# Optimization experiments

Hardware: AMD Instinct MI355X
Metric: run time of the kernel (lower is better)

The kernel has to match this reference:

```python
import jax, jax.numpy as jnp
import numpy as np

HIDDEN = 512
B, H, W = 8, 48, 48
SCALE = 1.0 / np.sqrt(HIDDEN).astype(np.float32)


def conv1x1(x, w, b):
    # x: [B, C, H, W], w: [O, C], b: [O]  (1x1 Conv2d == channel matmul)
    return jnp.einsum('bchw,oc->bohw', x, w) + b[None, :, None, None]


def setup_inputs() -> dict:
    key = jax.random.key(0)
    ks = jax.random.split(key, 10)
    s = 1.0 / np.sqrt(HIDDEN)
    return {
        'locx': jax.random.normal(ks[0], (B, HIDDEN, H, W), dtype=jnp.float32),
        'glox': jax.random.normal(ks[1], (B, HIDDEN, H, W), dtype=jnp.float32),
        'Wq': jax.random.normal(ks[2], (HIDDEN, HIDDEN), dtype=jnp.float32) * s,
        'bq': jax.random.normal(ks[3], (HIDDEN,), dtype=jnp.float32) * 0.01,
        'Wk': jax.random.normal(ks[4], (HIDDEN, HIDDEN), dtype=jnp.float32) * s,
        'bk': jax.random.normal(ks[5], (HIDDEN,), dtype=jnp.float32) * 0.01,
        'Wv': jax.random.normal(ks[6], (HIDDEN, HIDDEN), dtype=jnp.float32) * s,
        'bv': jax.random.normal(ks[7], (HIDDEN,), dtype=jnp.float32) * 0.01,
        'Wo': jax.random.normal(ks[8], (HIDDEN, HIDDEN), dtype=jnp.float32) * s,
        'bo': jax.random.normal(ks[9], (HIDDEN,), dtype=jnp.float32) * 0.01,
    }


def reference(locx, glox, Wq, bq, Wk, bk, Wv, bv, Wo, bo):
    b, c, h, w = locx.shape
    # 1x1 conv projections
    q = conv1x1(locx, Wq, bq).reshape(b, c, h * w)   # [B, C, N]
    k = conv1x1(glox, Wk, bk).reshape(b, c, -1)      # [B, C, M]
    v = conv1x1(glox, Wv, bv).reshape(b, c, -1)      # [B, C, M]
    # scores = Q^T K / sqrt(hidden)  -> [B, N, M]
    scores = jnp.einsum('bcn,bcm->bnm', q, k) * SCALE
    probs = jax.nn.softmax(scores, axis=-1)           # dropout rate 0.0 -> identity
    # context = probs @ V^T -> [B, N, C] -> [B, C, H, H]
    ctx = jnp.einsum('bnm,bcm->bcn', probs, v).reshape(b, c, h, h)
    out = conv1x1(ctx, Wo, bo)                        # proj dropout 0.0 -> identity
    return out
```

## Files before the change

### kernel.cpp

```cpp
#include <hip/hip_runtime.h>
#include <hip/hip_bf16.h>

typedef __attribute__((ext_vector_type(4))) float f32x4;
typedef __attribute__((ext_vector_type(8))) short bf16x8;
typedef __attribute__((ext_vector_type(4))) short s16x4;

#define C_DIM 512
#define N_PIX 2304
#define N_BATCH 8
#define ATT_SCALE 0.04419417382415922f
#define NJB 18

typedef __attribute__((address_space(3))) unsigned int lds_u32;
typedef const __attribute__((address_space(1))) unsigned int glob_u32;

__device__ __forceinline__ void gl2lds16(const __hip_bfloat16* g, __hip_bfloat16* l)
{
    __builtin_amdgcn_global_load_lds((glob_u32*)g, (lds_u32*)l, 16, 0, 0);
}

template<int OUT_BF16, int BIAS_MODE, int EPI, int MERGE2, int NJ, int NS>
__global__ __launch_bounds__(256)
void gemm_bt(const __hip_bfloat16* __restrict__ A0, const __hip_bfloat16* __restrict__ B0,
             void* __restrict__ D0, const float* __restrict__ bias0,
             float* __restrict__ rsum,
             const __hip_bfloat16* __restrict__ A1, const __hip_bfloat16* __restrict__ B1,
             void* __restrict__ D1, const float* __restrict__ bias1,
             float scale, int K, int lda, int ldb, int ldd,
             long sA, long sB, long sD)
{
    __shared__ __hip_bfloat16 As[128 * 64];
    __shared__ __hip_bfloat16 Bs[128 * 64];

    const int lin = blockIdx.x;
    const int s   = lin % NS;
    const int t   = lin / NS;
    const int bz  = MERGE2 ? (s & 7) : s;
    const int jb  = t % NJ;
    const int j0  = jb * 128;
    const int i0  = (t / NJ) * 128;

    const __hip_bfloat16* A = A0;
    const __hip_bfloat16* B = B0;
    void* Dp = (void*)D0;
    const float* bias = bias0;
    if (MERGE2 && (s >> 3)) { A = A1; B = B1; Dp = D1; bias = bias1; }

    const int tid  = threadIdx.x;
    const int lane = tid & 63;
    const int wave = tid >> 6;

    const __hip_bfloat16* Ab = A + (size_t)bz * (size_t)sA;
    const __hip_bfloat16* Bb = B + (size_t)bz * (size_t)sB;
    __hip_bfloat16* D16 = (__hip_bfloat16*)Dp + (size_t)bz * (size_t)sD;
    float*          D32 = (float*)Dp          + (size_t)bz * (size_t)sD;

    const int lrow = lane >> 3;
    const int lcs  = (lane & 7) ^ lrow;
    const __hip_bfloat16* ga = Ab + (size_t)(i0 + wave * 32 + lrow) * lda + lcs * 8;
    const __hip_bfloat16* gb = Bb + (size_t)(j0 + wave * 32 + lrow) * ldb + lcs * 8;
    __hip_bfloat16* la = As + wave * 32 * 64;
    __hip_bfloat16* lb = Bs + wave * 32 * 64;

    const int fr = lane & 15;
    const int fq = lane >> 4;
    const int sw = fr & 7;
    const int wi = (wave >> 1) * 64;
    const int wj = (wave & 1) * 64;

    f32x4 acc[4][4];
#pragma unroll
    for (int a = 0; a < 4; ++a)
#pragma unroll
        for (int b = 0; b < 4; ++b)
            acc[a][b] = (f32x4){0.f, 0.f, 0.f, 0.f};

    for (int k0 = 0; k0 < K; k0 += 64) {
#pragma unroll
        for (int ss = 0; ss < 4; ++ss) {
            gl2lds16(ga + (size_t)ss * 8 * lda + k0, la + ss * 8 * 64);
            gl2lds16(gb + (size_t)ss * 8 * ldb + k0, lb + ss * 8 * 64);
        }
        __syncthreads();

#pragma unroll
        for (int kk = 0; kk < 2; ++kk) {
            bf16x8 af[4], bfr[4];
            const int ca = ((kk * 4 + fq) ^ sw) << 3;
#pragma unroll
            for (int tt = 0; tt < 4; ++tt) {
                af[tt]  = *(const bf16x8*)(&As[(wi + tt * 16 + fr) * 64 + ca]);
                bfr[tt] = *(const bf16x8*)(&Bs[(wj + tt * 16 + fr) * 64 + ca]);
            }
#pragma unroll
            for (int a = 0; a < 4; ++a)
#pragma unroll
                for (int b = 0; b < 4; ++b)
                    acc[a][b] = __builtin_amdgcn_mfma_f32_16x16x32_bf16(
                        af[a], bfr[b], acc[a][b], 0, 0, 0);
        }
        __syncthreads();
    }

    const int orow = fq * 4;

    float inv[4][4];
    if (EPI == 2) {
        const float* ri = rsum + (size_t)bz * N_PIX;
#pragma unroll
        for (int a = 0; a < 4; ++a)
#pragma unroll
            for (int r = 0; r < 4; ++r)
                inv[a][r] = ri[i0 + wi + a * 16 + orow + r];
    }

    float rpart[4][4];
    if (EPI == 1) {
#pragma unroll
        for (int a = 0; a < 4; ++a)
#pragma unroll
            for (int r = 0; r < 4; ++r)
                rpart[a][r] = 0.f;
    }

#pragma unroll
    for (int a = 0; a < 4; ++a) {
        int ib = i0 + wi + a * 16 + orow;
#pragma unroll
        for (int b = 0; b < 4; ++b) {
            int j = j0 + wj + b * 16 + fr;
            float bj = (BIAS_MODE == 2) ? bias[j] : 0.f;
#pragma unroll
            for (int r = 0; r < 4; ++r) {
                int i = ib + r;
                float v = acc[a][b][r] * scale;
                if (BIAS_MODE == 1) v += bias[i];
                if (BIAS_MODE == 2) v += bj;
                if (EPI == 1) { v = __expf(v); rpart[a][r] += v; }
                if (EPI == 2) v *= inv[a][r];
                if (OUT_BF16)
                    D16[(size_t)i * ldd + j] = __float2bfloat16(v);
                else
                    D32[(size_t)i * ldd + j] = v;
            }
        }
    }

    if (EPI == 1) {
#pragma unroll
        for (int m = 1; m < 16; m <<= 1)
#pragma unroll
            for (int a = 0; a < 4; ++a)
#pragma unroll
                for (int r = 0; r < 4; ++r)
                    rpart[a][r] += __shfl_xor(rpart[a][r], m);
        float* rsl = (float*)As;
        if (fr == 0) {
#pragma unroll
            for (int a = 0; a < 4; ++a)
#pragma unroll
                for (int r = 0; r < 4; ++r)
                    rsl[wave * 64 + a * 16 + orow + r] = rpart[a][r];
        }
        __syncthreads();
        if (tid < 128) {
            int half = tid >> 6, rr = tid & 63;
            float sm = rsl[(half * 2) * 64 + rr] + rsl[(half * 2 + 1) * 64 + rr];
            rsum[((size_t)jb * N_BATCH + bz) * N_PIX + i0 + tid] = sm;
        }
    }
}

__global__ __launch_bounds__(256)
void reduce_rinv(const float* __restrict__ rp, float* __restrict__ rinv)
{
    int idx = blockIdx.x * 256 + threadIdx.x;
    float s = 0.f;
#pragma unroll
    for (int jb = 0; jb < NJB; ++jb)
        s += rp[(size_t)jb * N_BATCH * N_PIX + idx];
    rinv[idx] = 1.f / s;
}

__global__ __launch_bounds__(256)
void transpose_cast(const float* __restrict__ X, __hip_bfloat16* __restrict__ Xt)
{
    __shared__ float t[64 * 65];
    const int n0 = blockIdx.x * 64;
    const int c0 = blockIdx.y * 64;
    const size_t b = blockIdx.z;
    const float* Xb = X + b * (size_t)C_DIM * N_PIX;
    const int tid = threadIdx.x;

    const int n_l = tid & 63;
    const int c_b = tid >> 6;
#pragma unroll
    for (int s = 0; s < 16; ++s) {
        int c_l = c_b + s * 4;
        t[c_l * 65 + n_l] = Xb[(size_t)(c0 + c_l) * N_PIX + n0 + n_l];
    }
    __syncthreads();

    const int cc = (tid & 7) * 8;
    const int nb = tid >> 3;
#pragma unroll
    for (int it = 0; it < 2; ++it) {
        int n2 = nb + it * 32;
        union { __hip_bfloat16 h[8]; int4 v; } u;
#pragma unroll
        for (int w = 0; w < 8; ++w)
            u.h[w] = __float2bfloat16(t[(cc + w) * 65 + n2]);
        *(int4*)(&Xt[((size_t)b * N_PIX + n0 + n2) * C_DIM + c0 + cc]) = u.v;
    }
}

__global__ __launch_bounds__(256)
void cast_w4(const float* __restrict__ s0, const float* __restrict__ s1,
             const float* __restrict__ s2, const float* __restrict__ s3,
             __hip_bfloat16* __restrict__ dst)
{
    const float* srcs[4] = {s0, s1, s2, s3};
    const int w = blockIdx.y;
    const int i = (blockIdx.x * 256 + threadIdx.x) * 4;
    float4 f = *(const float4*)(srcs[w] + i);
    union { __hip_bfloat16 h[4]; s16x4 q; } t;
    t.h[0] = __float2bfloat16(f.x);
    t.h[1] = __float2bfloat16(f.y);
    t.h[2] = __float2bfloat16(f.z);
    t.h[3] = __float2bfloat16(f.w);
    *(s16x4*)(dst + (size_t)w * C_DIM * C_DIM + i) = t.q;
}

extern "C" void kernel_launch(void* const* d_in, const int* in_sizes, int n_in,
                              void* d_out, int out_size, void* d_ws, size_t ws_size,
                              hipStream_t stream)
{
    const float* locx = (const float*)d_in[0];
    const float* glox = (const float*)d_in[1];
    const float* Wq = (const float*)d_in[2];
    const float* bq = (const float*)d_in[3];
    const float* Wk = (const float*)d_in[4];
    const float* bk = (const float*)d_in[5];
    const float* Wv = (const float*)d_in[6];
    const float* bv = (const float*)d_in[7];
    const float* Wo = (const float*)d_in[8];
    const float* bo = (const float*)d_in[9];
    float* out = (float*)d_out;

    const int C = C_DIM, N = N_PIX;
    const size_t WB   = (size_t)C * C * 2;
    const size_t szX  = (size_t)N_BATCH * N * C * 2;
    const size_t szP1 = (size_t)N * N * 2;
    const size_t szRP = (size_t)NJB * N_BATCH * N * 4;
    const size_t szRI = (size_t)N_BATCH * N * 4;

    const size_t fixed = 4 * WB + 6 * szX + szRP + szRI;
    bool full = (ws_size >= fixed + 8 * szP1 + 8 * 256);

    char* ws = (char*)d_ws;
    size_t off = 0;
    auto alloc = [&](size_t bytes) {
        char* p = ws + off;
        off += (bytes + 255) & ~(size_t)255;
        return p;
    };
    __hip_bfloat16* wgt = (__hip_bfloat16*)alloc(4 * WB);
    __hip_bfloat16* Xl  = (__hip_bfloat16*)alloc(szX);
    __hip_bfloat16* Xg  = (__hip_bfloat16*)alloc(szX);
    __hip_bfloat16* Qt  = (__hip_bfloat16*)alloc(szX);
    __hip_bfloat16* Kt  = (__hip_bfloat16*)alloc(szX);
    __hip_bfloat16* Vb  = (__hip_bfloat16*)alloc(szX);
    __hip_bfloat16* Ctx = (__hip_bfloat16*)alloc(szX);
    float*          rp   = (float*)alloc(szRP);
    float*          rinv = (float*)alloc(szRI);
    __hip_bfloat16* Pu  = (__hip_bfloat16*)alloc(full ? 8 * szP1 : szP1);

    __hip_bfloat16* wq_b = wgt;
    __hip_bfloat16* wk_b = wgt + (size_t)C * C;
    __hip_bfloat16* wv_b = wgt + 2 * (size_t)C * C;
    __hip_bfloat16* wo_b = wgt + 3 * (size_t)C * C;

    const dim3 blk(256);
    const long sPr = (long)N * C;
    const long sV  = (long)C * N;

    cast_w4<<<dim3(C * C / 1024, 4), blk, 0, stream>>>(Wq, Wk, Wv, Wo, wgt);
    transpose_cast<<<dim3(N / 64, C / 64, 8), blk, 0, stream>>>(locx, Xl);
    transpose_cast<<<dim3(N / 64, C / 64, 8), blk, 0, stream>>>(glox, Xg);

    gemm_bt<1, 2, 0, 1, 4, 16><<<dim3(18 * 4 * 16), blk, 0, stream>>>(
        Xl, wq_b, Qt, bq, nullptr, Xg, wk_b, Kt, bk,
        1.f, C, C, C, C, sPr, 0, sPr);
    gemm_bt<1, 1, 0, 0, 18, 8><<<dim3(4 * 18 * 8), blk, 0, stream>>>(
        wv_b, Xg, Vb, bv, nullptr, nullptr, nullptr, nullptr, nullptr,
        1.f, C, C, C, N, 0, sPr, sV);

    if (full) {
        gemm_bt<1, 0, 1, 0, 18, 8><<<dim3(18 * 18 * 8), blk, 0, stream>>>(
            Qt, Kt, Pu, nullptr, rp, nullptr, nullptr, nullptr, nullptr,
            ATT_SCALE, C, C, C, N, sPr, sPr, (long)N * N);
        reduce_rinv<<<dim3(8 * N / 256), blk, 0, stream>>>(rp, rinv);
        gemm_bt<1, 0, 2, 0, 4, 8><<<dim3(18 * 4 * 8), blk, 0, stream>>>(
            Pu, Vb, Ctx, nullptr, rinv, nullptr, nullptr, nullptr, nullptr,
            1.f, N, N, N, C, (long)N * N, sV, sPr);
    } else {
        for (int r = 0; r < N_BATCH; ++r) {
            gemm_bt<1, 0, 1, 0, 18, 1><<<dim3(18 * 18), blk, 0, stream>>>(
                Qt + (size_t)r * sPr, Kt + (size_t)r * sPr, Pu, nullptr,
                rp + (size_t)r * N, nullptr, nullptr, nullptr, nullptr,
                ATT_SCALE, C, C, C, N, 0, 0, 0);
            reduce_rinv<<<dim3(N / 256), blk, 0, stream>>>(
                rp + (size_t)r * N, rinv + (size_t)r * N);
            gemm_bt<1, 0, 2, 0, 4, 1><<<dim3(18 * 4), blk, 0, stream>>>(
                Pu, Vb + (size_t)r * sV, Ctx + (size_t)r * sPr, nullptr,
                rinv + (size_t)r * N, nullptr, nullptr, nullptr, nullptr,
                1.f, N, N, N, C, 0, 0, 0);
        }
    }

    gemm_bt<0, 1, 0, 0, 18, 8><<<dim3(4 * 18 * 8), blk, 0, stream>>>(
        wo_b, Ctx, out, bo, nullptr, nullptr, nullptr, nullptr, nullptr,
        1.f, C, C, C, N, 0, sPr, (long)C * N);
}
```

Measured before the change: 368.2 us.

## Fold output projection into V before attention and fuse QKV projections

Uses associativity so Wo is applied to V first (Vp = Wo·V), and the final GEMM computes out = Vp·P^T with column-wise softmax normalization and bias applied in the epilogue. This removes the separate Ctx buffer and the final projection GEMM over the attention output. Q, K and V projections are merged into one kernel, and both input transposes run in a single launch, cutting launch count. Normalization now happens after the Wo product, which changes rounding order, and the P·V GEMM now writes fp32 output directly.

```diff
diff --git a/kernel.cpp b/kernel.cpp
--- a/kernel.cpp
+++ b/kernel.cpp
@@ -19,13 +19,11 @@
     __builtin_amdgcn_global_load_lds((glob_u32*)g, (lds_u32*)l, 16, 0, 0);
 }
 
-template<int OUT_BF16, int BIAS_MODE, int EPI, int MERGE2, int NJ, int NS>
+template<int OUT_BF16, int BIAS_MODE, int EPI, int NJ, int NS, int IFAST, int NI>
 __global__ __launch_bounds__(256)
-void gemm_bt(const __hip_bfloat16* __restrict__ A0, const __hip_bfloat16* __restrict__ B0,
-             void* __restrict__ D0, const float* __restrict__ bias0,
+void gemm_bt(const __hip_bfloat16* __restrict__ A, const __hip_bfloat16* __restrict__ B,
+             void* __restrict__ Dp, const float* __restrict__ bias,
              float* __restrict__ rsum,
-             const __hip_bfloat16* __restrict__ A1, const __hip_bfloat16* __restrict__ B1,
-             void* __restrict__ D1, const float* __restrict__ bias1,
              float scale, int K, int lda, int ldb, int ldd,
              long sA, long sB, long sD)
 {
@@ -35,16 +33,12 @@
     const int lin = blockIdx.x;
     const int s   = lin % NS;
     const int t   = lin / NS;
-    const int bz  = MERGE2 ? (s & 7) : s;
-    const int jb  = t % NJ;
-    const int j0  = jb * 128;
-    const int i0  = (t / NJ) * 128;
-
-    const __hip_bfloat16* A = A0;
-    const __hip_bfloat16* B = B0;
-    void* Dp = (void*)D0;
-    const float* bias = bias0;
-    if (MERGE2 && (s >> 3)) { A = A1; B = B1; Dp = D1; bias = bias1; }
+    const int bz  = s;
+    int ib, jb;
+    if (IFAST) { ib = t % NI; jb = t / NI; }
+    else       { jb = t % NJ; ib = t / NJ; }
+    const int i0 = ib * 128;
+    const int j0 = jb * 128;
 
     const int tid  = threadIdx.x;
     const int lane = tid & 63;
@@ -104,14 +98,12 @@
 
     const int orow = fq * 4;
 
-    float inv[4][4];
-    if (EPI == 2) {
+    float rjv[4];
+    if (EPI == 3) {
         const float* ri = rsum + (size_t)bz * N_PIX;
 #pragma unroll
-        for (int a = 0; a < 4; ++a)
-#pragma unroll
-            for (int r = 0; r < 4; ++r)
-                inv[a][r] = ri[i0 + wi + a * 16 + orow + r];
+        for (int b = 0; b < 4; ++b)
+            rjv[b] = ri[j0 + wj + b * 16 + fr];
     }
 
     float rpart[4][4];
@@ -125,19 +117,19 @@
 
 #pragma unroll
     for (int a = 0; a < 4; ++a) {
-        int ib = i0 + wi + a * 16 + orow;
+        int ibx = i0 + wi + a * 16 + orow;
 #pragma unroll
         for (int b = 0; b < 4; ++b) {
             int j = j0 + wj + b * 16 + fr;
             float bj = (BIAS_MODE == 2) ? bias[j] : 0.f;
 #pragma unroll
             for (int r = 0; r < 4; ++r) {
-                int i = ib + r;
+                int i = ibx + r;
                 float v = acc[a][b][r] * scale;
+                if (EPI == 3) v *= rjv[b];
                 if (BIAS_MODE == 1) v += bias[i];
                 if (BIAS_MODE == 2) v += bj;
                 if (EPI == 1) { v = __expf(v); rpart[a][r] += v; }
-                if (EPI == 2) v *= inv[a][r];
                 if (OUT_BF16)
                     D16[(size_t)i * ldd + j] = __float2bfloat16(v);
                 else
@@ -172,6 +164,96 @@
 }
 
 __global__ __launch_bounds__(256)
+void proj_qkv(const __hip_bfloat16* __restrict__ Xl,
+              const __hip_bfloat16* __restrict__ Xg,
+              const __hip_bfloat16* __restrict__ wgt,
+              const float* __restrict__ bq, const float* __restrict__ bk,
+              const float* __restrict__ bv,
+              __hip_bfloat16* __restrict__ QKV)
+{
+    __shared__ __hip_bfloat16 As[128 * 64];
+    __shared__ __hip_bfloat16 Bs[128 * 64];
+
+    const int lin = blockIdx.x;
+    const int s   = lin % 24;
+    const int bz  = s & 7;
+    const int mat = s >> 3;
+    const int t   = lin / 24;
+    const int j0  = (t & 3) * 128;
+    const int i0  = (t >> 2) * 128;
+
+    const __hip_bfloat16* Ab = ((mat == 0) ? Xl : Xg) + (size_t)bz * N_PIX * C_DIM;
+    const __hip_bfloat16* Bb = wgt + (size_t)mat * C_DIM * C_DIM;
+    const float* bias = (mat == 0) ? bq : (mat == 1) ? bk : bv;
+    __hip_bfloat16* D = QKV + ((size_t)mat * N_BATCH + bz) * N_PIX * C_DIM;
+
+    const int tid  = threadIdx.x;
+    const int lane = tid & 63;
+    const int wave = tid >> 6;
+
+    const int lrow = lane >> 3;
+    const int lcs  = (lane & 7) ^ lrow;
+    const __hip_bfloat16* ga = Ab + (size_t)(i0 + wave * 32 + lrow) * C_DIM + lcs * 8;
+    const __hip_bfloat16* gb = Bb + (size_t)(j0 + wave * 32 + lrow) * C_DIM + lcs * 8;
+    __hip_bfloat16* la = As + wave * 32 * 64;
+    __hip_bfloat16* lb = Bs + wave * 32 * 64;
+
+    const int fr = lane & 15;
+    const int fq = lane >> 4;
+    const int sw = fr & 7;
+    const int wi = (wave >> 1) * 64;
+    const int wj = (wave & 1) * 64;
+
+    f32x4 acc[4][4];
+#pragma unroll
+    for (int a = 0; a < 4; ++a)
+#pragma unroll
+        for (int b = 0; b < 4; ++b)
+            acc[a][b] = (f32x4){0.f, 0.f, 0.f, 0.f};
+
+    for (int k0 = 0; k0 < C_DIM; k0 += 64) {
+#pragma unroll
+        for (int ss = 0; ss < 4; ++ss) {
+            gl2lds16(ga + (size_t)ss * 8 * C_DIM + k0, la + ss * 8 * 64);
+            gl2lds16(gb + (size_t)ss * 8 * C_DIM + k0, lb + ss * 8 * 64);
+        }
+        __syncthreads();
+
+#pragma unroll
+        for (int kk = 0; kk < 2; ++kk) {
+            bf16x8 af[4], bfr[4];
+            const int ca = ((kk * 4 + fq) ^ sw) << 3;
+#pragma unroll
+            for (int tt = 0; tt < 4; ++tt) {
+                af[tt]  = *(const bf16x8*)(&As[(wi + tt * 16 + fr) * 64 + ca]);
+                bfr[tt] = *(const bf16x8*)(&Bs[(wj + tt * 16 + fr) * 64 + ca]);
+            }
+#pragma unroll
+            for (int a = 0; a < 4; ++a)
+#pragma unroll
+                for (int b = 0; b < 4; ++b)
+                    acc[a][b] = __builtin_amdgcn_mfma_f32_16x16x32_bf16(
+                        af[a], bfr[b], acc[a][b], 0, 0, 0);
+        }
+        __syncthreads();
+    }
+
+    const int orow = fq * 4;
+#pragma unroll
+    for (int a = 0; a < 4; ++a) {
+        int ibx = i0 + wi + a * 16 + orow;
+#pragma unroll
+        for (int b = 0; b < 4; ++b) {
+            int j = j0 + wj + b * 16 + fr;
+            float bj = bias[j];
+#pragma unroll
+            for (int r = 0; r < 4; ++r)
+                D[(size_t)(ibx + r) * C_DIM + j] = __float2bfloat16(acc[a][b][r] + bj);
+        }
+    }
+}
+
+__global__ __launch_bounds__(256)
 void reduce_rinv(const float* __restrict__ rp, float* __restrict__ rinv)
 {
     int idx = blockIdx.x * 256 + threadIdx.x;
@@ -183,13 +265,16 @@
 }
 
 __global__ __launch_bounds__(256)
-void transpose_cast(const float* __restrict__ X, __hip_bfloat16* __restrict__ Xt)
+void transpose_cast(const float* __restrict__ locx, const float* __restrict__ glox,
+                    __hip_bfloat16* __restrict__ Xl, __hip_bfloat16* __restrict__ Xg)
 {
     __shared__ float t[64 * 65];
     const int n0 = blockIdx.x * 64;
     const int c0 = blockIdx.y * 64;
-    const size_t b = blockIdx.z;
-    const float* Xb = X + b * (size_t)C_DIM * N_PIX;
+    const int z  = blockIdx.z;
+    const size_t b = z & 7;
+    const float* Xb = ((z < 8) ? locx : glox) + b * (size_t)C_DIM * N_PIX;
+    __hip_bfloat16* Xt = (z < 8) ? Xl : Xg;
     const int tid = threadIdx.x;
 
     const int n_l = tid & 63;
@@ -210,7 +295,7 @@
 #pragma unroll
         for (int w = 0; w < 8; ++w)
             u.h[w] = __float2bfloat16(t[(cc + w) * 65 + n2]);
-        *(int4*)(&Xt[((size_t)b * N_PIX + n0 + n2) * C_DIM + c0 + cc]) = u.v;
+        *(int4*)(&Xt[(b * N_PIX + n0 + n2) * C_DIM + c0 + cc]) = u.v;
     }
 }
 
@@ -255,7 +340,7 @@
     const size_t szRI = (size_t)N_BATCH * N * 4;
 
     const size_t fixed = 4 * WB + 6 * szX + szRP + szRI;
-    bool full = (ws_size >= fixed + 8 * szP1 + 8 * 256);
+    bool full = (ws_size >= fixed + 8 * szP1 + 4096);
 
     char* ws = (char*)d_ws;
     size_t off = 0;
@@ -267,58 +352,52 @@
     __hip_bfloat16* wgt = (__hip_bfloat16*)alloc(4 * WB);
     __hip_bfloat16* Xl  = (__hip_bfloat16*)alloc(szX);
     __hip_bfloat16* Xg  = (__hip_bfloat16*)alloc(szX);
-    __hip_bfloat16* Qt  = (__hip_bfloat16*)alloc(szX);
-    __hip_bfloat16* Kt  = (__hip_bfloat16*)alloc(szX);
-    __hip_bfloat16* Vb  = (__hip_bfloat16*)alloc(szX);
-    __hip_bfloat16* Ctx = (__hip_bfloat16*)alloc(szX);
+    __hip_bfloat16* QKV = (__hip_bfloat16*)alloc(3 * szX);
+    __hip_bfloat16* Vp  = (__hip_bfloat16*)alloc(szX);
     float*          rp   = (float*)alloc(szRP);
     float*          rinv = (float*)alloc(szRI);
     __hip_bfloat16* Pu  = (__hip_bfloat16*)alloc(full ? 8 * szP1 : szP1);
 
-    __hip_bfloat16* wq_b = wgt;
-    __hip_bfloat16* wk_b = wgt + (size_t)C * C;
-    __hip_bfloat16* wv_b = wgt + 2 * (size_t)C * C;
+    __hip_bfloat16* Qt = QKV;
+    __hip_bfloat16* Kt = QKV + (size_t)N_BATCH * N * C;
+    __hip_bfloat16* Vt = QKV + 2 * (size_t)N_BATCH * N * C;
     __hip_bfloat16* wo_b = wgt + 3 * (size_t)C * C;
 
     const dim3 blk(256);
     const long sPr = (long)N * C;
-    const long sV  = (long)C * N;
+    const long sCN = (long)C * N;
 
     cast_w4<<<dim3(C * C / 1024, 4), blk, 0, stream>>>(Wq, Wk, Wv, Wo, wgt);
-    transpose_cast<<<dim3(N / 64, C / 64, 8), blk, 0, stream>>>(locx, Xl);
-    transpose_cast<<<dim3(N / 64, C / 64, 8), blk, 0, stream>>>(glox, Xg);
-
-    gemm_bt<1, 2, 0, 1, 4, 16><<<dim3(18 * 4 * 16), blk, 0, stream>>>(
-        Xl, wq_b, Qt, bq, nullptr, Xg, wk_b, Kt, bk,
-        1.f, C, C, C, C, sPr, 0, sPr);
-    gemm_bt<1, 1, 0, 0, 18, 8><<<dim3(4 * 18 * 8), blk, 0, stream>>>(
-        wv_b, Xg, Vb, bv, nullptr, nullptr, nullptr, nullptr, nullptr,
-        1.f, C, C, C, N, 0, sPr, sV);
+    transpose_cast<<<dim3(N / 64, C / 64, 16), blk, 0, stream>>>(locx, glox, Xl, Xg);
+
+    proj_qkv<<<dim3(24 * 72), blk, 0, stream>>>(Xl, Xg, wgt, bq, bk, bv, QKV);
 
     if (full) {
-        gemm_bt<1, 0, 1, 0, 18, 8><<<dim3(18 * 18 * 8), blk, 0, stream>>>(
-            Qt, Kt, Pu, nullptr, rp, nullptr, nullptr, nullptr, nullptr,
+        gemm_bt<1, 0, 1, 18, 8, 0, 0><<<dim3(18 * 18 * 8), blk, 0, stream>>>(
+            Qt, Kt, Pu, nullptr, rp,
             ATT_SCALE, C, C, C, N, sPr, sPr, (long)N * N);
+        gemm_bt<1, 0, 0, 18, 8, 1, 4><<<dim3(4 * 18 * 8), blk, 0, stream>>>(
+            wo_b, Vt, Vp, nullptr, nullptr,
+            1.f, C, C, C, N, 0, sPr, sCN);
         reduce_rinv<<<dim3(8 * N / 256), blk, 0, stream>>>(rp, rinv);
-        gemm_bt<1, 0, 2, 0, 4, 8><<<dim3(18 * 4 * 8), blk, 0, stream>>>(
-            Pu, Vb, Ctx, nullptr, rinv, nullptr, nullptr, nullptr, nullptr,
-            1.f, N, N, N, C, (long)N * N, sV, sPr);
+        gemm_bt<0, 1, 3, 18, 8, 1, 4><<<dim3(4 * 18 * 8), blk, 0, stream>>>(
+            Vp, Pu, out, bo, rinv,
+            1.f, N, N, N, N, sCN, (long)N * N, sCN);
     } else {
+        gemm_bt<1, 0, 0, 18, 8, 1, 4><<<dim3(4 * 18 * 8), blk, 0, stream>>>(
+            wo_b, Vt, Vp, nullptr, nullptr,
+            1.f, C, C, C, N, 0, sPr, sCN);
         for (int r = 0; r < N_BATCH; ++r) {
-            gemm_bt<1, 0, 1, 0, 18, 1><<<dim3(18 * 18), blk, 0, stream>>>(
+            gemm_bt<1, 0, 1, 18, 1, 0, 0><<<dim3(18 * 18), blk, 0, stream>>>(
                 Qt + (size_t)r * sPr, Kt + (size_t)r * sPr, Pu, nullptr,
-                rp + (size_t)r * N, nullptr, nullptr, nullptr, nullptr,
+                rp + (size_t)r * N,
                 ATT_SCALE, C, C, C, N, 0, 0, 0);
             reduce_rinv<<<dim3(N / 256), blk, 0, stream>>>(
                 rp + (size_t)r * N, rinv + (size_t)r * N);
-            gemm_bt<1, 0, 2, 0, 4, 1><<<dim3(18 * 4), blk, 0, stream>>>(
-                Pu, Vb + (size_t)r * sV, Ctx + (size_t)r * sPr, nullptr,
-                rinv + (size_t)r * N, nullptr, nullptr, nullptr, nullptr,
-                1.f, N, N, N, C, 0, 0, 0);
-        }
-    }
-
-    gemm_bt<0, 1, 0, 0, 18, 8><<<dim3(4 * 18 * 8), blk, 0, stream>>>(
-        wo_b, Ctx, out, bo, nullptr, nullptr, nullptr, nullptr, nullptr,
-        1.f, C, C, C, N, 0, sPr, (long)C * N);
-}
+            gemm_bt<0, 1, 3, 18, 1, 1, 4><<<dim3(4 * 18), blk, 0, stream>>>(
+                Vp + (size_t)r * sCN, Pu, out + (size_t)r * sCN, bo,
+                rinv + (size_t)r * N,
+                1.f, N, N, N, N, 0, 0, 0);
+        }
+    }
+}
```

Result: faster. 339.8 us (-7.7%).
